# Kernel tuning notes

Hardware: AMD Instinct MI355X
Metric: run time of the kernel (lower is better)

The kernel has to match this reference:

```python
import jax, jax.numpy as jnp
import numpy as np

K = 5           # kernel_size
STRIDE = 1
DILATION = 1
PAD = 2         # padding='same': total = dilation*(K-1) = 4, left = 2, right = 2 (reflect mode)


def setup_inputs() -> dict:
    key = jax.random.key(0)
    k1, k2, k3, k4 = jax.random.split(key, 4)
    B, C_in, C_out, L = 8, 64, 64, 16384
    x = jax.random.normal(k1, (B, C_in, L), dtype=jnp.float32)
    # offsets broadcast over channels: (B, 1, L_out, K); L_out == L for padding='same'
    offsets = jax.random.normal(k2, (B, 1, L, K), dtype=jnp.float32)
    weight = jax.random.normal(k3, (C_out, C_in, K), dtype=jnp.float32) * (1.0 / np.sqrt(C_in * K))
    bias = jax.random.normal(k4, (C_out,), dtype=jnp.float32) * 0.05
    return {"x": x, "offsets": offsets, "weight": weight, "bias": bias}


def _deform_interp(xp, offsets):
    # xp: (B, C, Lp) padded input; offsets: (B, 1, Lo, K)
    B, C, Lp = xp.shape
    Lo, Kk = offsets.shape[-2], offsets.shape[-1]
    t0 = (STRIDE * jnp.arange(Lo, dtype=xp.dtype))[:, None]          # base sample positions
    dil = (DILATION * jnp.arange(Kk, dtype=xp.dtype))[None, :]       # dilated kernel positions
    T = jnp.clip(t0 + dil + offsets, 0.0, float(Lp - 1))             # (B, 1, Lo, K)
    i0 = jnp.clip(jnp.floor(T).astype(jnp.int32), 0, Lp - 2)
    frac = T - i0.astype(xp.dtype)                                   # linear-interp weight
    i0b = jnp.broadcast_to(i0, (B, C, Lo, Kk)).reshape(B, C, Lo * Kk)
    g0 = jnp.take_along_axis(xp, i0b, axis=-1).reshape(B, C, Lo, Kk)
    g1 = jnp.take_along_axis(xp, i0b + 1, axis=-1).reshape(B, C, Lo, Kk)
    return g0 * (1.0 - frac) + g1 * frac                             # (B, C, Lo, K)


def reference(x, offsets, weight, bias):
    # 'same' padding with reflect mode
    xp = jnp.pad(x, ((0, 0), (0, 0), (PAD, PAD)), mode="reflect")
    v = _deform_interp(xp, offsets)                                  # (B, C, Lo, K)
    # flatten(-2,-1) + conv1d(stride=K, groups=1) == contraction over (c, k) per output pos
    out = jnp.einsum("bclk,ock->bol", v, weight) + bias[None, :, None]
    return out
```

## Files before the change

### kernel.cpp

```cpp
#include <hip/hip_runtime.h>

#define BATCH 8
#define CIN   64
#define COUT  64
#define LEN   16384
#define KS    5
#define PADW  2
#define LP    (LEN + 2*PADW)
#define TTB   128
#define XROWS 104
#define XM    14

typedef __attribute__((ext_vector_type(8)))  short short8;
typedef __attribute__((ext_vector_type(4)))  float f32x4;
typedef __attribute__((ext_vector_type(8)))  unsigned short ushort8;

__device__ __forceinline__ unsigned short bf16r(float f) {
    unsigned u = __builtin_bit_cast(unsigned, f);
    u += 0x7FFF + ((u >> 16) & 1);
    return (unsigned short)(u >> 16);
}
__device__ __forceinline__ int reflmap(int s) {
    return (s < PADW) ? (PADW - s) : ((s < LEN + PADW) ? (s - PADW) : (2*LEN - s));
}

__global__ void wfrag_kernel(const float* __restrict__ w, unsigned short* __restrict__ wf) {
    int el = blockIdx.x * 256 + threadIdx.x;
    int e    = el & 7;
    int lane = (el >> 3) & 63;
    int kk   = (el >> 9) % 10;
    int ot   = el / 5120;
    int o    = ot * 16 + (lane & 15);
    int kg   = kk * 32 + ((lane >> 4) << 3) + e;
    int ktap = kg >> 6;
    int c    = kg & 63;
    wf[el] = bf16r(w[(o * 64 + c) * 5 + ktap]);
}

__global__ __launch_bounds__(256, 4) void deform_mfma_kernel(
    const float* __restrict__ x, const float* __restrict__ offs,
    const unsigned short* __restrict__ wf, const float* __restrict__ bias,
    float* __restrict__ out)
{
    __shared__ __align__(16) unsigned short xtl[2][XROWS * 64];

    const int tid = threadIdx.x;
    const int bid = blockIdx.x;
    const int bt  = (bid & 7) * 128 + (bid >> 3);
    const int b   = bt >> 7;
    const int T0  = (bt & 127) * TTB;
    const int w   = tid >> 6;
    const int lane = tid & 63;
    const int pl  = lane & 15;
    const int s   = lane >> 4;

    const float* xb0 = x + (size_t)b * CIN * LEN;
    const unsigned short* wfl = wf + (size_t)lane * 8;

    float of[2][KS];
    #pragma unroll
    for (int it = 0; it < 2; ++it) {
        const int tc = T0 + it * 64 + w * 16 + pl;
        #pragma unroll
        for (int k = 0; k < KS; ++k)
            of[it][k] = offs[((size_t)(b * LEN + tc)) * KS + k];
    }

    float4 sA[4], sB[4];
    int stg_fast;

#define STAGE_LOAD(t0s)                                                        \
    stg_fast = ((t0s) >= 16 && (t0s) + 88 <= LEN);                             \
    if (stg_fast) {                                                            \
        const float* src0 = xb0 + ((t0s) - 16);                                \
        _Pragma("unroll")                                                      \
        for (int rep = 0; rep < 4; ++rep) {                                    \
            int task = rep * 256 + tid;           \
            if (task < 832) {                                                  \
                int c = task / 13, q = task - c * 13;                          \
                const float* p = src0 + (size_t)c * LEN + 8 * q;               \
                sA[rep] = *(const float4*)p;                                   \
                sB[rep] = *(const float4*)(p + 4);                             \
            }                                                                  \
        }                                                                      \
    }

#define STAGE_WRITE(dst, t0s)                                                  \
    if (stg_fast) {                                                            \
        _Pragma("unroll")                                                      \
        for (int rep = 0; rep < 4; ++rep) {                                    \
            int task = rep * 256 + tid;                                        \
            if (task < 832) {                                                  \
                int c = task / 13, q = task - c * 13;                          \
                float vv[8] = {sA[rep].x, sA[rep].y, sA[rep].z, sA[rep].w,     \
                               sB[rep].x, sB[rep].y, sB[rep].z, sB[rep].w};    \
                _Pragma("unroll")                                              \
                for (int i = 0; i < 8; ++i) {                                  \
                    int r = 8 * q + i;                                         \
                    *(unsigned short*)((char*)(dst) + r * 128 +                \
                        ((2 * c) ^ ((r & 7) << 4))) = bf16r(vv[i]);            \
                }                                                              \
            }                                                                  \
        }                                                                      \
    } else {                                                                   \
        const int S0e = (t0s) - XM;                                            \
        _Pragma("unroll")                                                      \
        for (int rep = 0; rep < 26; ++rep) {                                   \
            int idx = rep * 256 + tid;                    \
            int r = idx >> 6, c = idx & 63;                                    \
            int sp = min(max(S0e + r, 0), LP - 1);                             \
            *(unsigned short*)((char*)(dst) + r * 128 +                        \
                ((2 * c) ^ ((r & 7) << 4))) = bf16r(xb0[(size_t)c * LEN + reflmap(sp)]); \
        }                                                                      \
    }

#define LERPP(pk, j, w0, w1, f)                                                \
    {                                                                          \
        float g0a = __builtin_bit_cast(float, (w0) << 16);                     \
        float g1a = __builtin_bit_cast(float, (w1) << 16);                     \
        float g0b = __builtin_bit_cast(float, (w0) & 0xFFFF0000u);             \
        float g1b = __builtin_bit_cast(float, (w1) & 0xFFFF0000u);             \
        pk[2*(j)]   = bf16r(fmaf(f, g1a - g0a, g0a));                          \
        pk[2*(j)+1] = bf16r(fmaf(f, g1b - g0b, g0b));                          \
    }

#define GST(kk, CHECKED)                                                       \
    {                                                                          \
        const int k = (kk) >> 1;                                               \
        const int m = (((kk) & 1) << 2) + s;                   \
        const float f = frr[k];                                                \
        ushort8 pk;                                                            \
        if (!(CHECKED) || (unsigned)r0r[k] <= (unsigned)(XROWS - 2)) {         \
            const int r0 = r0r[k], r1 = r0r[k] + 1;                            \
            uint4 u0 = *(const uint4*)((const char*)xbuf + r0 * 128 + ((m * 16) ^ ((r0 & 7) << 4))); \
            uint4 u1 = *(const uint4*)((const char*)xbuf + r1 * 128 + ((m * 16) ^ ((r1 & 7) << 4))); \
            LERPP(pk, 0, u0.x, u1.x, f) LERPP(pk, 1, u0.y, u1.y, f)            \
            LERPP(pk, 2, u0.z, u1.z, f) LERPP(pk, 3, u0.w, u1.w, f)            \
        } else {                                                               \
            int j0 = reflmap(i0r[k]), j1 = reflmap(i0r[k] + 1);                \
            const float* xc = xb0 + (size_t)(m << 3) * LEN;                    \
            _Pragma("unroll")                                                  \
            for (int e = 0; e < 8; ++e) {                                      \
                float g0 = xc[j0], g1 = xc[j1];                                \
                pk[e] = bf16r(fmaf(f, g1 - g0, g0));                           \
                xc += LEN;                                                     \
            }                                                                  \
        }                                                                      \
        short8 bv = __builtin_bit_cast(short8, pk);                            \
        short8 a0 = *(const short8*)&wfl[(0 * 10 + (kk)) * 512];               \
        short8 a1 = *(const short8*)&wfl[(1 * 10 + (kk)) * 512];               \
        short8 a2 = *(const short8*)&wfl[(2 * 10 + (kk)) * 512];               \
        short8 a3 = *(const short8*)&wfl[(3 * 10 + (kk)) * 512];               \
        acc0 = __builtin_amdgcn_mfma_f32_16x16x32_bf16(a0, bv, acc0, 0, 0, 0); \
        acc1 = __builtin_amdgcn_mfma_f32_16x16x32_bf16(a1, bv, acc1, 0, 0, 0); \
        acc2 = __builtin_amdgcn_mfma_f32_16x16x32_bf16(a2, bv, acc2, 0, 0, 0); \
        acc3 = __builtin_amdgcn_mfma_f32_16x16x32_bf16(a3, bv, acc3, 0, 0, 0); \
    }

#define SUBTILE(it)                                                            \
    {                                                                          \
        const int t0s = T0 + (it) * 64;                                        \
        if ((it) == 0) { STAGE_LOAD(t0s + 64); }    \
        const int S0 = t0s - XM;                                               \
        const int tc = t0s + w * 16 + pl;                                      \
        int i0r[KS]; float frr[KS]; int r0r[KS]; bool fastg = true;            \
        _Pragma("unroll")                                                      \
        for (int k = 0; k < KS; ++k) {                                         \
            float T = (float)(tc + k) + of[it][k];                             \
            T = fminf(fmaxf(T, 0.0f), (float)(LP - 1));                        \
            int i0 = (int)floorf(T);                                           \
            i0 = min(i0, LP - 2); i0 = max(i0, 0);                             \
            i0r[k] = i0; frr[k] = T - (float)i0; r0r[k] = i0 - S0;             \
            fastg = fastg && ((unsigned)(i0 - S0) <= (unsigned)(XROWS - 2));   \
        }                                                                      \
        const unsigned short* xbuf = xtl[(it)];                                \
        f32x4 acc0 = {}, acc1 = {}, acc2 = {}, acc3 = {};                      \
        if (fastg) { GST(0,0) GST(1,0) GST(2,0) GST(3,0) GST(4,0)              \
                     GST(5,0) GST(6,0) GST(7,0) GST(8,0) GST(9,0) }            \
        else       { GST(0,1) GST(1,1) GST(2,1) GST(3,1) GST(4,1)              \
                     GST(5,1) GST(6,1) GST(7,1) GST(8,1) GST(9,1) }            \
        _Pragma("unroll")                                                      \
        for (int ot = 0; ot < 4; ++ot) {                                       \
            const f32x4 a = (ot==0)?acc0:(ot==1)?acc1:(ot==2)?acc2:acc3;       \
            _Pragma("unroll")                                                  \
            for (int r = 0; r < 4; ++r) {                                      \
                int o = ot * 16 + s * 4 + r;                                   \
                out[((size_t)(b * COUT + o)) * LEN + tc] = a[r] + bias[o];     \
            }                                                                  \
        }                                                                      \
        if ((it) == 0) { STAGE_WRITE(xtl[1], t0s + 64); __syncthreads(); }     \
    }

    STAGE_LOAD(T0);
    STAGE_WRITE(xtl[0], T0);
    __syncthreads();

    SUBTILE(0)
    SUBTILE(1)

#undef SUBTILE
#undef GST
#undef LERPP
#undef STAGE_WRITE
#undef STAGE_LOAD
}

extern "C" void kernel_launch(void* const* d_in, const int* in_sizes, int n_in,
                              void* d_out, int out_size, void* d_ws, size_t ws_size,
                              hipStream_t stream) {
    const float* x    = (const float*)d_in[0];
    const float* offs = (const float*)d_in[1];
    const float* w    = (const float*)d_in[2];
    const float* bias = (const float*)d_in[3];
    float* out = (float*)d_out;
    unsigned short* wf = (unsigned short*)d_ws;

    wfrag_kernel<<<80, 256, 0, stream>>>(w, wf);
    deform_mfma_kernel<<<BATCH * (LEN / TTB), 256, 0, stream>>>(x, offs, wf, bias, out);
}
```

Baseline: 38.15 us.

## Software-pipeline LDS gathers ahead of MFMA compute and simplify block mapping

Splits the fast-path gather into separate load and compute macros and issues LDS loads several steps ahead of the lerp+MFMA work, so shared-memory latency overlaps with math. The slow path becomes a fully global-memory fallback with no per-tap range check. The block-index swizzle that interleaved batches across consecutive blocks is dropped in favour of a linear mapping. Holding up to 20 uint4 values raises register pressure, which could hurt occupancy under launch_bounds(256,4).

```diff
diff --git a/kernel.cpp b/kernel.cpp
--- a/kernel.cpp
+++ b/kernel.cpp
@@ -45,8 +45,7 @@
     __shared__ __align__(16) unsigned short xtl[2][XROWS * 64];
 
     const int tid = threadIdx.x;
-    const int bid = blockIdx.x;
-    const int bt  = (bid & 7) * 128 + (bid >> 3);
+    const int bt  = blockIdx.x;
     const int b   = bt >> 7;
     const int T0  = (bt & 127) * TTB;
     const int w   = tid >> 6;
@@ -124,28 +123,20 @@
         pk[2*(j)+1] = bf16r(fmaf(f, g1b - g0b, g0b));                          \
     }
 
-#define GST(kk, CHECKED)                                                       \
-    {                                                                          \
-        const int k = (kk) >> 1;                                               \
-        const int m = (((kk) & 1) << 2) + s;                   \
-        const float f = frr[k];                                                \
+#define GLOAD(kk)                                                              \
+    {                                                                          \
+        const int r0 = r0r[(kk) >> 1], r1 = r0 + 1;                            \
+        const int mm = ((((kk) & 1) << 2) + s) * 16;                           \
+        U0[kk] = *(const uint4*)((const char*)xbuf + r0 * 128 + (mm ^ ((r0 & 7) << 4))); \
+        U1[kk] = *(const uint4*)((const char*)xbuf + r1 * 128 + (mm ^ ((r1 & 7) << 4))); \
+    }
+
+#define GCOMP(kk)                                                              \
+    {                                                                          \
+        const float f = frr[(kk) >> 1];                                        \
         ushort8 pk;                                                            \
-        if (!(CHECKED) || (unsigned)r0r[k] <= (unsigned)(XROWS - 2)) {         \
-            const int r0 = r0r[k], r1 = r0r[k] + 1;                            \
-            uint4 u0 = *(const uint4*)((const char*)xbuf + r0 * 128 + ((m * 16) ^ ((r0 & 7) << 4))); \
-            uint4 u1 = *(const uint4*)((const char*)xbuf + r1 * 128 + ((m * 16) ^ ((r1 & 7) << 4))); \
-            LERPP(pk, 0, u0.x, u1.x, f) LERPP(pk, 1, u0.y, u1.y, f)            \
-            LERPP(pk, 2, u0.z, u1.z, f) LERPP(pk, 3, u0.w, u1.w, f)            \
-        } else {                                                               \
-            int j0 = reflmap(i0r[k]), j1 = reflmap(i0r[k] + 1);                \
-            const float* xc = xb0 + (size_t)(m << 3) * LEN;                    \
-            _Pragma("unroll")                                                  \
-            for (int e = 0; e < 8; ++e) {                                      \
-                float g0 = xc[j0], g1 = xc[j1];                                \
-                pk[e] = bf16r(fmaf(f, g1 - g0, g0));                           \
-                xc += LEN;                                                     \
-            }                                                                  \
-        }                                                                      \
+        LERPP(pk, 0, U0[kk].x, U1[kk].x, f) LERPP(pk, 1, U0[kk].y, U1[kk].y, f)\
+        LERPP(pk, 2, U0[kk].z, U1[kk].z, f) LERPP(pk, 3, U0[kk].w, U1[kk].w, f)\
         short8 bv = __builtin_bit_cast(short8, pk);                            \
         short8 a0 = *(const short8*)&wfl[(0 * 10 + (kk)) * 512];               \
         short8 a1 = *(const short8*)&wfl[(1 * 10 + (kk)) * 512];               \
@@ -157,6 +148,31 @@
         acc3 = __builtin_amdgcn_mfma_f32_16x16x32_bf16(a3, bv, acc3, 0, 0, 0); \
     }
 
+#define GSLOW(kk)                                                              \
+    {                                                                          \
+        const int k = (kk) >> 1;                                               \
+        const int m = (((kk) & 1) << 2) + s;                                   \
+        const float f = frr[k];                                                \
+        ushort8 pk;                                                            \
+        int j0 = reflmap(i0r[k]), j1 = reflmap(i0r[k] + 1);                    \
+        const float* xc = xb0 + (size_t)(m << 3) * LEN;                        \
+        _Pragma("unroll")                                                      \
+        for (int e = 0; e < 8; ++e) {                                          \
+            float g0 = xc[j0], g1 = xc[j1];                                    \
+            pk[e] = bf16r(fmaf(f, g1 - g0, g0));                               \
+            xc += LEN;                                                         \
+        }                                                                      \
+        short8 bv = __builtin_bit_cast(short8, pk);                            \
+        short8 a0 = *(const short8*)&wfl[(0 * 10 + (kk)) * 512];               \
+        short8 a1 = *(const short8*)&wfl[(1 * 10 + (kk)) * 512];               \
+        short8 a2 = *(const short8*)&wfl[(2 * 10 + (kk)) * 512];               \
+        short8 a3 = *(const short8*)&wfl[(3 * 10 + (kk)) * 512];               \
+        acc0 = __builtin_amdgcn_mfma_f32_16x16x32_bf16(a0, bv, acc0, 0, 0, 0); \
+        acc1 = __builtin_amdgcn_mfma_f32_16x16x32_bf16(a1, bv, acc1, 0, 0, 0); \
+        acc2 = __builtin_amdgcn_mfma_f32_16x16x32_bf16(a2, bv, acc2, 0, 0, 0); \
+        acc3 = __builtin_amdgcn_mfma_f32_16x16x32_bf16(a3, bv, acc3, 0, 0, 0); \
+    }
+
 #define SUBTILE(it)                                                            \
     {                                                                          \
         const int t0s = T0 + (it) * 64;                                        \
@@ -175,10 +191,16 @@
         }                                                                      \
         const unsigned short* xbuf = xtl[(it)];                                \
         f32x4 acc0 = {}, acc1 = {}, acc2 = {}, acc3 = {};                      \
-        if (fastg) { GST(0,0) GST(1,0) GST(2,0) GST(3,0) GST(4,0)              \
-                     GST(5,0) GST(6,0) GST(7,0) GST(8,0) GST(9,0) }            \
-        else       { GST(0,1) GST(1,1) GST(2,1) GST(3,1) GST(4,1)              \
-                     GST(5,1) GST(6,1) GST(7,1) GST(8,1) GST(9,1) }            \
+        if (fastg) {                                                           \
+            uint4 U0[10], U1[10];                                              \
+            GLOAD(0) GLOAD(1) GLOAD(2) GLOAD(3) GLOAD(4)                       \
+            GCOMP(0) GLOAD(5) GCOMP(1) GLOAD(6) GCOMP(2) GLOAD(7)              \
+            GCOMP(3) GLOAD(8) GCOMP(4) GLOAD(9)                                \
+            GCOMP(5) GCOMP(6) GCOMP(7) GCOMP(8) GCOMP(9)                       \
+        } else {                                                               \
+            GSLOW(0) GSLOW(1) GSLOW(2) GSLOW(3) GSLOW(4)                       \
+            GSLOW(5) GSLOW(6) GSLOW(7) GSLOW(8) GSLOW(9)                       \
+        }                                                                      \
         _Pragma("unroll")                                                      \
         for (int ot = 0; ot < 4; ++ot) {                                       \
             const f32x4 a = (ot==0)?acc0:(ot==1)?acc1:(ot==2)?acc2:acc3;       \
@@ -199,7 +221,9 @@
     SUBTILE(1)
 
 #undef SUBTILE
-#undef GST
+#undef GSLOW
+#undef GCOMP
+#undef GLOAD
 #undef LERPP
 #undef STAGE_WRITE
 #undef STAGE_LOAD
```

After: 44.68 us. +17.1%, slower.
